# Optimization experiments

Hardware: AMD Instinct MI355X
Metric: run time of the kernel (lower is better)

## Reference

```python
import jax, jax.numpy as jnp
import numpy as np

B, T, D, H = 4, 2048, 1024, 16
E = D // H  # 64
DH = D // 4  # sensor hidden dim


def setup_inputs() -> dict:
    key = jax.random.key(0)
    ks = jax.random.split(key, 9)
    s = D ** -0.5
    return {
        "x": jax.random.normal(ks[0], (B, T, D), jnp.float32),
        "q_w": jax.random.normal(ks[1], (D, D), jnp.float32) * s,
        "k_w": jax.random.normal(ks[2], (D, D), jnp.float32) * s,
        "v_w": jax.random.normal(ks[3], (D, D), jnp.float32) * s,
        "o_w": jax.random.normal(ks[4], (D, D), jnp.float32) * s,
        "cs_w1": jax.random.normal(ks[5], (DH, D), jnp.float32) * s,
        "cs_b1": jnp.zeros((DH,), jnp.float32),
        "cs_w2": jax.random.normal(ks[6], (H, DH), jnp.float32) * (DH ** -0.5),
        "cs_b2": jnp.zeros((H,), jnp.float32),
        "decay_params": jax.random.normal(ks[7], (H, E), jnp.float32) + 3.0,
    }


def reference(x, q_w, k_w, v_w, o_w, cs_w1, cs_b1, cs_w2, cs_b2, decay_params):
    Bx, Tx, Dx = x.shape
    # projections (torch Linear: y = x @ W.T), split into heads
    q = (x @ q_w.T).reshape(Bx, Tx, H, E)
    k = (x @ k_w.T).reshape(Bx, Tx, H, E)
    v = (x @ v_w.T).reshape(Bx, Tx, H, E)
    # complexity sensor -> per-head scalar in (0,1)
    lc = jax.nn.sigmoid(jnp.tanh(x @ cs_w1.T + cs_b1) @ cs_w2.T + cs_b2)  # [B,T,H]
    base = jax.nn.sigmoid(decay_params)[None, None]                       # [1,1,H,E]
    lam = jnp.clip(base * (1.0 + 0.2 * lc[..., None]), 0.0, 0.9995)       # [B,T,H,E]

    def step(state, inp):
        qt, kt, vt, dt = inp  # each [B,H,E]
        # S(t) = diag(dt) S(t-1) + k_t v_t^T  (decay along key dim e)
        state = state * dt[..., None] + kt[..., None] * vt[:, :, None, :]
        out_t = jnp.einsum('bhe,bhef->bhf', qt, state)
        return state, out_t

    init = jnp.zeros((Bx, H, E, E), x.dtype)
    xs = (jnp.swapaxes(q, 0, 1), jnp.swapaxes(k, 0, 1),
          jnp.swapaxes(v, 0, 1), jnp.swapaxes(lam, 0, 1))  # time-major
    _, ys = jax.lax.scan(step, init, xs)  # ys: [T,B,H,E]
    y = jnp.swapaxes(ys, 0, 1).reshape(Bx, Tx, Dx)
    return y @ o_w.T
```

## Files before the change

kernel.cpp:

```cpp
#include <hip/hip_runtime.h>

#define DEV __device__ __forceinline__
#define MFMA(a, b, c) __builtin_amdgcn_mfma_f32_16x16x32_bf16(a, b, c, 0, 0, 0)

typedef __bf16 bf16x8 __attribute__((ext_vector_type(8)));
typedef float f32x4 __attribute__((ext_vector_type(4)));
typedef unsigned short u16x8 __attribute__((ext_vector_type(8)));

DEV float blo(unsigned u) { return __builtin_bit_cast(float, u << 16); }
DEV float bhi(unsigned u) { return __builtin_bit_cast(float, u & 0xFFFF0000u); }
DEV unsigned short f2b(float f) {
  unsigned u = __builtin_bit_cast(unsigned, f);
  return (unsigned short)((u + 0x7FFFu + ((u >> 16) & 1u)) >> 16);
}
DEV float sigf(float x) { return 1.0f / (1.0f + expf(-x)); }

DEV void llds16(const void* g, void* l) {
  __builtin_amdgcn_global_load_lds(
      (__attribute__((address_space(1))) void*)(void*)g,
      (__attribute__((address_space(3))) void*)l, 16, 0, 0);
}

__global__ __launch_bounds__(256) void cvt_all_kernel(
    const float* __restrict__ x, const float* __restrict__ qw,
    const float* __restrict__ kw, const float* __restrict__ vw,
    const float* __restrict__ cw1, const float* __restrict__ ow,
    unsigned short* __restrict__ XB, unsigned short* __restrict__ WCAT,
    unsigned short* __restrict__ OWB) {
  const int i = blockIdx.x * 256 + threadIdx.x;
  const float* s;
  unsigned short* d;
  if (i < 2097152)      { s = x   + (size_t)i * 4;                 d = XB + (size_t)i * 4; }
  else if (i < 2359296) { size_t j = i - 2097152; s = qw  + j * 4; d = WCAT + j * 4; }
  else if (i < 2621440) { size_t j = i - 2359296; s = kw  + j * 4; d = WCAT + 1048576 + j * 4; }
  else if (i < 2883584) { size_t j = i - 2621440; s = vw  + j * 4; d = WCAT + 2097152 + j * 4; }
  else if (i < 2949120) { size_t j = i - 2883584; s = cw1 + j * 4; d = WCAT + 3145728 + j * 4; }
  else if (i < 3211264) { size_t j = i - 2949120; s = ow  + j * 4; d = OWB + j * 4; }
  else return;
  float4 f = *(const float4*)s;
  ushort4 o;
  o.x = f2b(f.x); o.y = f2b(f.y); o.z = f2b(f.z); o.w = f2b(f.w);
  *(ushort4*)d = o;
}

template <int OUTF>
__global__ __launch_bounds__(256, 2) void gemm_bk64_kernel(
    const unsigned short* __restrict__ A, const unsigned short* __restrict__ B,
    void* __restrict__ Cout, unsigned short* __restrict__ Cout2,
    int K, int ldC, int act_col0, const float* __restrict__ bias, int nbn) {
  __shared__ char As[16384];
  __shared__ char Bs[16384];
  const int tid = threadIdx.x;
  const int lane = tid & 63;
  const int w = tid >> 6;
  const int wr = w >> 1, wc = w & 1;
  const int ln15 = lane & 15, hi = lane >> 4;

  const int nwg = gridDim.x, orig = blockIdx.x;
  const int qd = nwg >> 3, rm = nwg & 7;
  const int xcd = orig & 7, loc = orig >> 3;
  const int swz = (xcd < rm ? xcd * (qd + 1) : rm * (qd + 1) + (xcd - rm) * qd) + loc;
  const int bn = swz % nbn, bm = swz / nbn;
  const int m0 = bm * 128, n0 = bn * 128;

  auto stage = [&](const unsigned short* src, int row0, int k0, char* dst) {
#pragma unroll
    for (int j = 0; j < 4; ++j) {
      const int slot = j * 256 + tid;
      const int rr = slot >> 3;
      const int kc = (slot & 7) ^ (rr & 7);
      llds16(src + (size_t)(row0 + rr) * K + k0 + kc * 8, dst + slot * 16);
    }
  };
  auto rd = [&](const char* unit, int row, int ks) -> bf16x8 {
    const int kc = (ks * 4 + hi) ^ (row & 7);
    return *(const bf16x8*)(unit + row * 128 + kc * 16);
  };

  f32x4 acc[4][4] = {};
  const int nk = K >> 6;
  for (int kt = 0; kt < nk; ++kt) {
    stage(A, m0, kt * 64, As);
    stage(B, n0, kt * 64, Bs);
    __syncthreads();
    bf16x8 af[2][4], bf[2][4];
#pragma unroll
    for (int ks = 0; ks < 2; ++ks)
#pragma unroll
      for (int i = 0; i < 4; ++i) {
        af[ks][i] = rd(As, wr * 64 + i * 16 + ln15, ks);
        bf[ks][i] = rd(Bs, wc * 64 + i * 16 + ln15, ks);
      }
#pragma unroll
    for (int i = 0; i < 4; ++i)
#pragma unroll
      for (int j = 0; j < 4; ++j) {
        acc[i][j] = MFMA(af[0][i], bf[0][j], acc[i][j]);
        acc[i][j] = MFMA(af[1][i], bf[1][j], acc[i][j]);
      }
    __syncthreads();
  }
#pragma unroll
  for (int i = 0; i < 4; ++i) {
    const int rowb = m0 + wr * 64 + i * 16 + hi * 4;
#pragma unroll
    for (int j = 0; j < 4; ++j) {
      const int col = n0 + wc * 64 + j * 16 + ln15;
#pragma unroll
      for (int r = 0; r < 4; ++r) {
        float v = acc[i][j][r];
        if (col >= act_col0) {
          v = tanhf(v + bias[col - act_col0]);
          Cout2[(size_t)(rowb + r) * 256 + (col - act_col0)] = f2b(v);
        } else {
          const size_t off = (size_t)(rowb + r) * ldC + col;
          if (OUTF == 0) ((unsigned short*)Cout)[off] = f2b(v);
          else ((float*)Cout)[off] = v;
        }
      }
    }
  }
}

__global__ __launch_bounds__(256) void sensor2_kernel(
    const unsigned short* __restrict__ H1, const float* __restrict__ w2,
    const float* __restrict__ b2, float* __restrict__ LC) {
  const int tid = threadIdx.x;
  const int h = tid & 15, r = tid >> 4;
  const int m = blockIdx.x * 16 + r;
  const unsigned short* hrow = H1 + (size_t)m * 256;
  const float* wrow = w2 + h * 256;
  float acc = 0.0f;
  for (int d = 0; d < 256; d += 8) {
    uint4 hv = *(const uint4*)(hrow + d);
    float4 wa = *(const float4*)(wrow + d);
    float4 wb = *(const float4*)(wrow + d + 4);
    acc = fmaf(blo(hv.x), wa.x, acc); acc = fmaf(bhi(hv.x), wa.y, acc);
    acc = fmaf(blo(hv.y), wa.z, acc); acc = fmaf(bhi(hv.y), wa.w, acc);
    acc = fmaf(blo(hv.z), wb.x, acc); acc = fmaf(bhi(hv.z), wb.y, acc);
    acc = fmaf(blo(hv.w), wb.z, acc); acc = fmaf(bhi(hv.w), wb.w, acc);
  }
  LC[(size_t)m * 16 + h] = sigf(acc + b2[h]);
}

__global__ __launch_bounds__(256) void scan_passA_kernel(
    const unsigned short* __restrict__ QKV, const float* __restrict__ LC,
    const float* __restrict__ decay, unsigned short* __restrict__ MTB,
    float* __restrict__ P) {
  __shared__ char SH[34304];
  ushort* kL = (ushort*)SH;
  ushort* vL = (ushort*)(SH + 8192);
  char* khT  = SH + 16384;
  char* vT   = SH + 24576;
  float* sigL = (float*)(SH + 32768);
  float* lcL  = (float*)(SH + 33024);
  float* Lp   = (float*)(SH + 33280);

  const int tid = threadIdx.x;
  const int c = blockIdx.x, h = blockIdx.y, b = blockIdx.z;
  const int t0 = c * 64;
#pragma unroll
  for (int i = 0; i < 2; ++i) {
    int idx = i * 256 + tid;
    int row = idx >> 3, ch = idx & 7;
    size_t g = (size_t)(b * 2048 + t0 + row) * 3072 + h * 64 + ch * 8;
    int lb = (i * 256 + (tid >> 6) * 64) * 16;
    llds16(QKV + g + 1024, (char*)kL + lb);
    llds16(QKV + g + 2048, (char*)vL + lb);
  }
  if (tid < 64) sigL[tid] = sigf(decay[h * 64 + tid]);
  else if (tid < 128) lcL[tid - 64] = LC[(size_t)(b * 2048 + t0 + tid - 64) * 16 + h];
  __syncthreads();

  const int e = tid & 63, seg = tid >> 6;
  const float sig_e = sigL[e];
  float lp = 1.f;
#pragma unroll
  for (int i = 0; i < 16; ++i)
    lp *= fminf(sig_e * (1.f + 0.2f * lcL[seg * 16 + i]), 0.9995f);
  Lp[seg * 64 + e] = lp;
  __syncthreads();
  float T = 1.f;
#pragma unroll
  for (int sg = 0; sg < 4; ++sg) if (sg > seg) T *= Lp[sg * 64 + e];

  u16x8 ka = {}, kb = {};
  float r = T;
#pragma unroll
  for (int i = 15; i >= 0; --i) {
    int s = seg * 16 + i;
    float lam = fminf(sig_e * (1.f + 0.2f * lcL[s]), 0.9995f);
    float kv = blo((unsigned)kL[s * 64 + e]) * r;
    if (i >= 8) kb[i - 8] = f2b(kv); else ka[i] = f2b(kv);
    r *= lam;
  }
  *(u16x8*)(khT + e * 128 + (((2 * seg + 0) ^ (e & 7)) * 16)) = ka;
  *(u16x8*)(khT + e * 128 + (((2 * seg + 1) ^ (e & 7)) * 16)) = kb;
  if (seg == 0) P[((size_t)((b * 16 + h) * 32 + c)) * 64 + e] = r;

  u16x8 va = {}, vb = {};
#pragma unroll
  for (int i = 0; i < 16; ++i) {
    unsigned short vv = vL[(seg * 16 + i) * 64 + e];
    if (i >= 8) vb[i - 8] = vv; else va[i] = vv;
  }
  *(u16x8*)(vT + e * 128 + (((2 * seg + 0) ^ (e & 7)) * 16)) = va;
  *(u16x8*)(vT + e * 128 + (((2 * seg + 1) ^ (e & 7)) * 16)) = vb;
  __syncthreads();

  const int ln15 = tid & 15, hi = (tid & 63) >> 4, w = tid >> 6;
  auto rd = [&](const char* u, int row, int ks) -> bf16x8 {
    return *(const bf16x8*)(u + row * 128 + (((ks * 4 + hi) ^ (row & 7)) * 16));
  };
  bf16x8 av0 = rd(vT, w * 16 + ln15, 0), av1 = rd(vT, w * 16 + ln15, 1);
  unsigned short* Mp = MTB + ((size_t)((b * 16 + h) * 32 + c)) * 4096;
#pragma unroll
  for (int er = 0; er < 4; ++er) {
    f32x4 acc = {};
    acc = MFMA(av0, rd(khT, er * 16 + ln15, 0), acc);
    acc = MFMA(av1, rd(khT, er * 16 + ln15, 1), acc);
    const int e2 = er * 16 + ln15;
#pragma unroll
    for (int rr = 0; rr < 4; ++rr) {
      const int f = w * 16 + hi * 4 + rr;
      Mp[f * 64 + (((e2 >> 3) ^ (f & 7)) << 3) + (e2 & 7)] = f2b(acc[rr]);
    }
  }
}

__global__ __launch_bounds__(256) void scan_passB_kernel(
    unsigned short* __restrict__ MTB, const float* __restrict__ P) {
  const int bh = blockIdx.y;
  const int task = blockIdx.x * 256 + threadIdx.x;
  const int f = task >> 6, slot = (task >> 3) & 7, pos = task & 7;
  const int e = ((slot ^ (f & 7)) << 3) | pos;
  const size_t base = (size_t)bh * 32;
  float S = 0.0f;
  for (int c = 0; c < 32; ++c) {
    unsigned short* Mp = MTB + (base + c) * 4096 + task;
    const float p = P[(base + c) * 64 + e];
    const float m = blo((unsigned)*Mp);
    *Mp = f2b(S);
    S = fmaf(p, S, m);
  }
}

__global__ __launch_bounds__(256) void scan_passC_kernel(
    const unsigned short* __restrict__ QKV, const float* __restrict__ LC,
    const float* __restrict__ decay, const unsigned short* __restrict__ MTB,
    unsigned short* __restrict__ Y) {
  __shared__ char SH[50688];
  ushort* qL = (ushort*)SH;
  ushort* kL = (ushort*)(SH + 8192);
  ushort* vL = (ushort*)(SH + 16384);
  char* qT = SH + 24576;
  char* kT = SH + 32768;
  char* vT = SH + 40960;
  char* Ab   = SH;
  char* sinT = SH + 8192;
  float* sigL = (float*)(SH + 49152);
  float* lcL  = (float*)(SH + 49408);
  float* Lp   = (float*)(SH + 49664);

  const int tid = threadIdx.x;
  const int c = blockIdx.x, h = blockIdx.y, b = blockIdx.z;
  const int t0 = c * 64;
#pragma unroll
  for (int i = 0; i < 2; ++i) {
    int idx = i * 256 + tid;
    int row = idx >> 3, ch = idx & 7;
    size_t g = (size_t)(b * 2048 + t0 + row) * 3072 + h * 64 + ch * 8;
    int lb = (i * 256 + (tid >> 6) * 64) * 16;
    llds16(QKV + g,        (char*)qL + lb);
    llds16(QKV + g + 1024, (char*)kL + lb);
    llds16(QKV + g + 2048, (char*)vL + lb);
  }
  if (tid < 64) sigL[tid] = sigf(decay[h * 64 + tid]);
  else if (tid < 128) lcL[tid - 64] = LC[(size_t)(b * 2048 + t0 + tid - 64) * 16 + h];
  __syncthreads();

  const int e = tid & 63, seg = tid >> 6;
  const float sig_e = sigL[e];
  float lp = 1.f;
#pragma unroll
  for (int i = 0; i < 16; ++i)
    lp *= fminf(sig_e * (1.f + 0.2f * lcL[seg * 16 + i]), 0.9995f);
  Lp[seg * 64 + e] = lp;
  __syncthreads();
  float a = 1.f;
#pragma unroll
  for (int sg = 0; sg < 4; ++sg) if (sg < seg) a *= Lp[sg * 64 + e];

#pragma unroll
  for (int i = 0; i < 16; ++i) {
    int t = seg * 16 + i;
    a *= fminf(sig_e * (1.f + 0.2f * lcL[t]), 0.9995f);
    float qv = blo((unsigned)qL[t * 64 + e]) * a;
    float kv = blo((unsigned)kL[t * 64 + e]) / fmaxf(a, 1e-30f);
    int off = ((e >> 3) ^ (t & 7)) * 16 + (e & 7) * 2;
    *(unsigned short*)(qT + t * 128 + off) = f2b(qv);
    *(unsigned short*)(kT + t * 128 + off) = f2b(kv);
  }
  u16x8 va = {}, vb = {};
#pragma unroll
  for (int i = 0; i < 16; ++i) {
    unsigned short vv = vL[(seg * 16 + i) * 64 + e];
    if (i >= 8) vb[i - 8] = vv; else va[i] = vv;
  }
  *(u16x8*)(vT + e * 128 + (((2 * seg + 0) ^ (e & 7)) * 16)) = va;
  *(u16x8*)(vT + e * 128 + (((2 * seg + 1) ^ (e & 7)) * 16)) = vb;
  __syncthreads();

  {
    const unsigned short* Ms = MTB + ((size_t)((b * 16 + h) * 32 + c)) * 4096;
#pragma unroll
    for (int i = 0; i < 2; ++i)
      llds16(Ms + (size_t)(i * 256 + tid) * 8, sinT + (i * 256 + (tid >> 6) * 64) * 16);
  }
  const int ln15 = tid & 15, hi = (tid & 63) >> 4, w = tid >> 6;
  auto rd = [&](const char* u, int row, int ks) -> bf16x8 {
    return *(const bf16x8*)(u + row * 128 + (((ks * 4 + hi) ^ (row & 7)) * 16));
  };
  bf16x8 Aq0 = rd(qT, w * 16 + ln15, 0), Aq1 = rd(qT, w * 16 + ln15, 1);
  f32x4 acc1[4];
#pragma unroll
  for (int sr = 0; sr < 4; ++sr) {
    acc1[sr] = (f32x4){0.f, 0.f, 0.f, 0.f};
    if (sr <= w) {
      acc1[sr] = MFMA(Aq0, rd(kT, sr * 16 + ln15, 0), acc1[sr]);
      acc1[sr] = MFMA(Aq1, rd(kT, sr * 16 + ln15, 1), acc1[sr]);
    }
  }
#pragma unroll
  for (int sr = 0; sr < 4; ++sr)
#pragma unroll
    for (int rr = 0; rr < 4; ++rr) {
      int t = w * 16 + hi * 4 + rr;
      int s = sr * 16 + ln15;
      float v = 0.f;
      if (sr <= w && s <= t) v = acc1[sr][rr];
      *(unsigned short*)(Ab + t * 128 + (((s >> 3) ^ (t & 7)) * 16) + (s & 7) * 2) = f2b(v);
    }
  bf16x8 Aa0 = rd(Ab, w * 16 + ln15, 0), Aa1 = rd(Ab, w * 16 + ln15, 1);
  __syncthreads();

  f32x4 accY[4];
#pragma unroll
  for (int fr = 0; fr < 4; ++fr) {
    accY[fr] = (f32x4){0.f, 0.f, 0.f, 0.f};
    accY[fr] = MFMA(Aq0, rd(sinT, fr * 16 + ln15, 0), accY[fr]);
    accY[fr] = MFMA(Aq1, rd(sinT, fr * 16 + ln15, 1), accY[fr]);
    accY[fr] = MFMA(Aa0, rd(vT, fr * 16 + ln15, 0), accY[fr]);
    accY[fr] = MFMA(Aa1, rd(vT, fr * 16 + ln15, 1), accY[fr]);
  }
#pragma unroll
  for (int fr = 0; fr < 4; ++fr)
#pragma unroll
    for (int rr = 0; rr < 4; ++rr)
      Y[(size_t)(b * 2048 + t0 + w * 16 + hi * 4 + rr) * 1024 + h * 64 + fr * 16 + ln15]
        = f2b(accY[fr][rr]);
}

extern "C" void kernel_launch(void* const* d_in, const int* in_sizes, int n_in,
                              void* d_out, int out_size, void* d_ws, size_t ws_size,
                              hipStream_t stream) {
  (void)in_sizes; (void)n_in; (void)out_size; (void)ws_size;
  const float* x     = (const float*)d_in[0];
  const float* q_w   = (const float*)d_in[1];
  const float* k_w   = (const float*)d_in[2];
  const float* v_w   = (const float*)d_in[3];
  const float* o_w   = (const float*)d_in[4];
  const float* cs_w1 = (const float*)d_in[5];
  const float* cs_b1 = (const float*)d_in[6];
  const float* cs_w2 = (const float*)d_in[7];
  const float* cs_b2 = (const float*)d_in[8];
  const float* decay = (const float*)d_in[9];
  float* out = (float*)d_out;

  char* ws = (char*)d_ws;
  unsigned short* XB   = (unsigned short*)(ws);
  unsigned short* WCAT = (unsigned short*)(ws + 16777216);
  unsigned short* OWB  = (unsigned short*)(ws + 23592960);
  unsigned short* QKV  = (unsigned short*)(ws + 25690112);
  unsigned short* H1   = (unsigned short*)(ws + 76021760);
  float*          LCb  = (float*)(ws + 80216064);
  unsigned short* MTB  = (unsigned short*)(ws + 80740352);
  float*          Pb   = (float*)(ws + 97517568);
  unsigned short* YB   = (unsigned short*)(ws + 98041856);

  cvt_all_kernel<<<12544, 256, 0, stream>>>(x, q_w, k_w, v_w, cs_w1, o_w,
                                            XB, WCAT, OWB);

  gemm_bk64_kernel<0><<<1664, 256, 0, stream>>>(XB, WCAT, QKV, H1,
                                                1024, 3072, 3072, cs_b1, 26);
  sensor2_kernel<<<512, 256, 0, stream>>>(H1, cs_w2, cs_b2, LCb);

  scan_passA_kernel<<<dim3(32, 16, 4), 256, 0, stream>>>(QKV, LCb, decay, MTB, Pb);
  scan_passB_kernel<<<dim3(16, 64), 256, 0, stream>>>(MTB, Pb);
  scan_passC_kernel<<<dim3(32, 16, 4), 256, 0, stream>>>(QKV, LCb, decay, MTB, YB);

  gemm_bk64_kernel<1><<<512, 256, 0, stream>>>(YB, OWB, out, nullptr,
                                               1024, 1024, 1 << 30, nullptr, 8);
}
```

Measured before the change: 169.6 us.

## Enlarge GEMM M-tile to 256 rows and replace per-step division in scan

```diff
diff --git a/kernel.cpp b/kernel.cpp
--- a/kernel.cpp
+++ b/kernel.cpp
@@ -44,16 +44,15 @@
 }
 
 template <int OUTF>
-__global__ __launch_bounds__(256, 2) void gemm_bk64_kernel(
+__global__ __launch_bounds__(256, 2) void gemm_bt256_kernel(
     const unsigned short* __restrict__ A, const unsigned short* __restrict__ B,
     void* __restrict__ Cout, unsigned short* __restrict__ Cout2,
     int K, int ldC, int act_col0, const float* __restrict__ bias, int nbn) {
-  __shared__ char As[16384];
+  __shared__ char As[32768];
   __shared__ char Bs[16384];
   const int tid = threadIdx.x;
   const int lane = tid & 63;
   const int w = tid >> 6;
-  const int wr = w >> 1, wc = w & 1;
   const int ln15 = lane & 15, hi = lane >> 4;
 
   const int nwg = gridDim.x, orig = blockIdx.x;
@@ -61,51 +60,56 @@
   const int xcd = orig & 7, loc = orig >> 3;
   const int swz = (xcd < rm ? xcd * (qd + 1) : rm * (qd + 1) + (xcd - rm) * qd) + loc;
   const int bn = swz % nbn, bm = swz / nbn;
-  const int m0 = bm * 128, n0 = bn * 128;
-
-  auto stage = [&](const unsigned short* src, int row0, int k0, char* dst) {
+  const int m0 = bm * 256, n0 = bn * 128;
+
+  auto rd = [&](const char* unit, int row, int ks) -> bf16x8 {
+    const int kc = (ks * 4 + hi) ^ (row & 7);
+    return *(const bf16x8*)(unit + row * 128 + kc * 16);
+  };
+
+  f32x4 acc[4][8] = {};
+  const int nk = K >> 6;
+  for (int kt = 0; kt < nk; ++kt) {
+    const int k0 = kt * 64;
+#pragma unroll
+    for (int j = 0; j < 8; ++j) {
+      const int slot = j * 256 + tid;
+      const int rr = slot >> 3;
+      const int kc = (slot & 7) ^ (rr & 7);
+      llds16(A + (size_t)(m0 + rr) * K + k0 + kc * 8, As + slot * 16);
+    }
 #pragma unroll
     for (int j = 0; j < 4; ++j) {
       const int slot = j * 256 + tid;
       const int rr = slot >> 3;
       const int kc = (slot & 7) ^ (rr & 7);
-      llds16(src + (size_t)(row0 + rr) * K + k0 + kc * 8, dst + slot * 16);
-    }
-  };
-  auto rd = [&](const char* unit, int row, int ks) -> bf16x8 {
-    const int kc = (ks * 4 + hi) ^ (row & 7);
-    return *(const bf16x8*)(unit + row * 128 + kc * 16);
-  };
-
-  f32x4 acc[4][4] = {};
-  const int nk = K >> 6;
-  for (int kt = 0; kt < nk; ++kt) {
-    stage(A, m0, kt * 64, As);
-    stage(B, n0, kt * 64, Bs);
+      llds16(B + (size_t)(n0 + rr) * K + k0 + kc * 8, Bs + slot * 16);
+    }
     __syncthreads();
-    bf16x8 af[2][4], bf[2][4];
+    bf16x8 af[2][4];
 #pragma unroll
     for (int ks = 0; ks < 2; ++ks)
 #pragma unroll
+      for (int i = 0; i < 4; ++i)
+        af[ks][i] = rd(As, w * 64 + i * 16 + ln15, ks);
+#pragma unroll
+    for (int j = 0; j < 8; ++j) {
+      bf16x8 b0 = rd(Bs, j * 16 + ln15, 0);
+      bf16x8 b1 = rd(Bs, j * 16 + ln15, 1);
+#pragma unroll
       for (int i = 0; i < 4; ++i) {
-        af[ks][i] = rd(As, wr * 64 + i * 16 + ln15, ks);
-        bf[ks][i] = rd(Bs, wc * 64 + i * 16 + ln15, ks);
+        acc[i][j] = MFMA(af[0][i], b0, acc[i][j]);
+        acc[i][j] = MFMA(af[1][i], b1, acc[i][j]);
       }
-#pragma unroll
-    for (int i = 0; i < 4; ++i)
-#pragma unroll
-      for (int j = 0; j < 4; ++j) {
-        acc[i][j] = MFMA(af[0][i], bf[0][j], acc[i][j]);
-        acc[i][j] = MFMA(af[1][i], bf[1][j], acc[i][j]);
-      }
+    }
     __syncthreads();
   }
 #pragma unroll
   for (int i = 0; i < 4; ++i) {
-    const int rowb = m0 + wr * 64 + i * 16 + hi * 4;
-#pragma unroll
-    for (int j = 0; j < 4; ++j) {
-      const int col = n0 + wc * 64 + j * 16 + ln15;
+    const int rowb = m0 + w * 64 + i * 16 + hi * 4;
+#pragma unroll
+    for (int j = 0; j < 8; ++j) {
+      const int col = n0 + j * 16 + ln15;
 #pragma unroll
       for (int r = 0; r < 4; ++r) {
         float v = acc[i][j][r];
@@ -281,24 +285,36 @@
 
   const int e = tid & 63, seg = tid >> 6;
   const float sig_e = sigL[e];
+  float lam[16];
+#pragma unroll
+  for (int i = 0; i < 16; ++i)
+    lam[i] = fminf(sig_e * (1.f + 0.2f * lcL[seg * 16 + i]), 0.9995f);
   float lp = 1.f;
 #pragma unroll
-  for (int i = 0; i < 16; ++i)
-    lp *= fminf(sig_e * (1.f + 0.2f * lcL[seg * 16 + i]), 0.9995f);
+  for (int i = 0; i < 16; ++i) lp *= lam[i];
   Lp[seg * 64 + e] = lp;
   __syncthreads();
   float a = 1.f;
 #pragma unroll
   for (int sg = 0; sg < 4; ++sg) if (sg < seg) a *= Lp[sg * 64 + e];
 
+  float ap = a;
 #pragma unroll
   for (int i = 0; i < 16; ++i) {
     int t = seg * 16 + i;
-    a *= fminf(sig_e * (1.f + 0.2f * lcL[t]), 0.9995f);
-    float qv = blo((unsigned)qL[t * 64 + e]) * a;
-    float kv = blo((unsigned)kL[t * 64 + e]) / fmaxf(a, 1e-30f);
+    ap *= lam[i];
+    float qv = blo((unsigned)qL[t * 64 + e]) * ap;
     int off = ((e >> 3) ^ (t & 7)) * 16 + (e & 7) * 2;
     *(unsigned short*)(qT + t * 128 + off) = f2b(qv);
+  }
+  const float inv_end = 1.0f / ap;
+  float R = 1.f;
+#pragma unroll
+  for (int i = 15; i >= 0; --i) {
+    int t = seg * 16 + i;
+    float kv = blo((unsigned)kL[t * 64 + e]) * (R * inv_end);
+    R *= lam[i];
+    int off = ((e >> 3) ^ (t & 7)) * 16 + (e & 7) * 2;
     *(unsigned short*)(kT + t * 128 + off) = f2b(kv);
   }
   u16x8 va = {}, vb = {};
@@ -391,7 +407,7 @@
   cvt_all_kernel<<<12544, 256, 0, stream>>>(x, q_w, k_w, v_w, cs_w1, o_w,
                                             XB, WCAT, OWB);
 
-  gemm_bk64_kernel<0><<<1664, 256, 0, stream>>>(XB, WCAT, QKV, H1,
+  gemm_bt256_kernel<0><<<832, 256, 0, stream>>>(XB, WCAT, QKV, H1,
                                                 1024, 3072, 3072, cs_b1, 26);
   sensor2_kernel<<<512, 256, 0, stream>>>(H1, cs_w2, cs_b2, LCb);
 
@@ -399,6 +415,6 @@
   scan_passB_kernel<<<dim3(16, 64), 256, 0, stream>>>(MTB, Pb);
   scan_passC_kernel<<<dim3(32, 16, 4), 256, 0, stream>>>(QKV, LCb, decay, MTB, YB);
 
-  gemm_bk64_kernel<1><<<512, 256, 0, stream>>>(YB, OWB, out, nullptr,
-                                               1024, 1024, 1 << 30, nullptr, 8);
-}
+  gemm_bt256_kernel<1><<<256, 256, 0, stream>>>(YB, OWB, out, nullptr,
+                                                1024, 1024, 1 << 30, nullptr, 8);
+}
```

Result: slower. 210.8 us (+24.3%).
